# Kernel optimization log

Hardware: AMD Instinct MI355X
Metric: run time of the kernel (lower is better)

The kernel has to match this reference:

```python
import jax, jax.numpy as jnp
import numpy as np

D, E, H, K = 1024, 8, 1024, 2          # d_model, num_experts, hidden_size, top_k
NUM_LAYERS, LB_W, Z_W = 16, 0.01, 0.001
B, S = 2, 2048


def setup_inputs() -> dict:
    key = jax.random.key(0)
    ks = jax.random.split(key, 8)
    s = lambda d: 1.0 / np.sqrt(d)
    return {
        "x": jax.random.normal(ks[0], (B, S, D), jnp.float32),
        "w_router": jax.random.normal(ks[1], (D, E), jnp.float32) * s(D),
        "w1": jax.random.normal(ks[2], (E, D, H), jnp.float32) * s(D),
        "w3": jax.random.normal(ks[3], (E, D, H), jnp.float32) * s(D),
        "w2": jax.random.normal(ks[4], (E, H, D), jnp.float32) * s(H),
        "sw1": jax.random.normal(ks[5], (D, H), jnp.float32) * s(D),
        "sw3": jax.random.normal(ks[6], (D, H), jnp.float32) * s(D),
        "sw2": jax.random.normal(ks[7], (H, D), jnp.float32) * s(H),
    }


def reference(x, w_router, w1, w3, w2, sw1, sw3, sw2):
    b, s_len, _ = x.shape
    xt = x.reshape(-1, D)                       # (N, D) flattened tokens
    n_tok = xt.shape[0]

    # ---- router: softmax over experts, then top-k ----
    logits = xt @ w_router                      # (N, E)
    probs = jax.nn.softmax(logits, axis=-1)
    weights, indices = jax.lax.top_k(probs, K)  # (N, K)

    # combine weights scattered back to dense (N, E) form
    onehot = jax.nn.one_hot(indices, E, dtype=x.dtype)    # (N, K, E)
    cw = jnp.einsum("nk,nke->ne", weights, onehot)       # (N, E)
    counts = jnp.sum(onehot, axis=(0, 1))                 # (E,) tokens per expert

    # ---- expert SwiGLU MLPs (dense dispatch, weighted combine) ----
    g = jnp.einsum("nd,edh->neh", xt, w1)                 # (N, E, H)
    u = jnp.einsum("nd,edh->neh", xt, w3)
    h = jax.nn.silu(g) * u
    eout = jnp.einsum("neh,ehd->ned", h, w2)              # (N, E, D)
    out = jnp.einsum("ne,ned->nd", cw, eout)              # (N, D)

    # ---- shared expert, weighted-sum combine with top_k ----
    shared = (jax.nn.silu(xt @ sw1) * (xt @ sw3)) @ sw2   # (N, D)
    out = (out * K + shared) / (K + 1)

    # ---- aux losses (training mode) ----
    logits32 = logits.astype(jnp.float32)
    scale = E * LB_W / (NUM_LAYERS * n_tok * K)
    lb_loss = scale * jnp.dot(counts.astype(jnp.float32),
                              jax.nn.softmax(logits32, axis=-1).sum(axis=0))
    z_loss = jnp.mean(jnp.square(jax.nn.logsumexp(logits32, axis=-1))) * Z_W

    return out.reshape(b, s_len, D), lb_loss, z_loss
```

## Files before the change

### kernel.cpp

```cpp
#include <hip/hip_runtime.h>

#define NTOK 4096
#define NEXP 8
#define MAXTILES 104

typedef __attribute__((ext_vector_type(8))) short short8;
typedef __attribute__((ext_vector_type(4))) float f32x4;
typedef __attribute__((ext_vector_type(4))) unsigned int uint4v;
typedef __attribute__((ext_vector_type(2))) unsigned int uint2v;

__device__ __forceinline__ unsigned short f2bf(float f) {
  union { float f; unsigned u; } v; v.f = f;
  unsigned u = v.u;
  return (unsigned short)((u + 0x7FFFu + ((u >> 16) & 1u)) >> 16);
}

__device__ __forceinline__ void gll16(const void* g, void* l) {
  __builtin_amdgcn_global_load_lds((const __attribute__((address_space(1))) void*)g,
                                   (__attribute__((address_space(3))) void*)l, 16, 0, 0);
}

__device__ __forceinline__ void transpose_tile(const float* __restrict__ S,
                                               unsigned short* __restrict__ Dp,
                                               int r0, int c0, int t,
                                               unsigned short (*tile)[65]) {
  int r = t >> 2, cb = (t & 3) * 16;
  const float* sp = S + (size_t)(r0 + r) * 1024 + c0 + cb;
  f32x4 v0 = ((const f32x4*)sp)[0], v1 = ((const f32x4*)sp)[1];
  f32x4 v2 = ((const f32x4*)sp)[2], v3 = ((const f32x4*)sp)[3];
#pragma unroll
  for (int j = 0; j < 4; ++j) {
    tile[r][cb + j] = f2bf(v0[j]);
    tile[r][cb + 4 + j] = f2bf(v1[j]);
    tile[r][cb + 8 + j] = f2bf(v2[j]);
    tile[r][cb + 12 + j] = f2bf(v3[j]);
  }
  __syncthreads();
  unsigned short* dp = Dp + (size_t)(c0 + r) * 1024 + r0 + cb;
  uint4v o0, o1;
#pragma unroll
  for (int j = 0; j < 4; ++j) {
    o0[j] = (unsigned)tile[cb + 2 * j][r] | ((unsigned)tile[cb + 2 * j + 1][r] << 16);
    o1[j] = (unsigned)tile[cb + 8 + 2 * j][r] | ((unsigned)tile[cb + 9 + 2 * j][r] << 16);
  }
  ((uint4v*)dp)[0] = o0;
  ((uint4v*)dp)[1] = o1;
}

__global__ __launch_bounds__(256) void prep_k(
    const float* __restrict__ w1, const float* __restrict__ w3,
    const float* __restrict__ sw1, const float* __restrict__ sw3,
    unsigned short* __restrict__ dst ,
    const float* __restrict__ x, const float* __restrict__ wr, unsigned short* __restrict__ xb,
    int* __restrict__ rec, float* __restrict__ wts, float* __restrict__ probs,
    float* __restrict__ lsebuf) {
  __shared__ unsigned short tile[64][65];
  int b = blockIdx.x;
  if (b < 4608) {
    int z = b >> 8, rem = b & 255;
    const float* S;
    unsigned short* Dp;
    if (z < 8) { S = w1 + (size_t)z * 1048576; Dp = dst + (size_t)z * 1048576; }
    else if (z < 16) { S = w3 + (size_t)(z - 8) * 1048576; Dp = dst + (size_t)z * 1048576; }
    else if (z == 16) { S = sw1; Dp = dst + (size_t)24 * 1048576; }
    else { S = sw3; Dp = dst + (size_t)25 * 1048576; }
    transpose_tile(S, Dp, (rem >> 4) * 64, (rem & 15) * 64, threadIdx.x, tile);
  } else {
    int t = threadIdx.x, lane = t & 63, wv = t >> 6;
    int tok = (b - 4608) * 4 + wv;
    const f32x4* x4 = (const f32x4*)(x + (size_t)tok * 1024);
    f32x4 xv[4];
#pragma unroll
    for (int j = 0; j < 4; ++j) xv[j] = x4[j * 64 + lane];

    unsigned short* xo = xb + (size_t)tok * 1024;
#pragma unroll
    for (int j = 0; j < 4; ++j) {
      uint2v o;
      o[0] = (unsigned)f2bf(xv[j][0]) | ((unsigned)f2bf(xv[j][1]) << 16);
      o[1] = (unsigned)f2bf(xv[j][2]) | ((unsigned)f2bf(xv[j][3]) << 16);
      *(uint2v*)(xo + j * 256 + lane * 4) = o;
    }

    float acc[NEXP];
#pragma unroll
    for (int e = 0; e < NEXP; ++e) acc[e] = 0.f;
#pragma unroll
    for (int j = 0; j < 4; ++j) {
      int base = j * 256 + lane * 4;
#pragma unroll
      for (int c = 0; c < 4; ++c) {
        float xf = xv[j][c];
        const f32x4* wp = (const f32x4*)(wr + (size_t)(base + c) * NEXP);
        f32x4 q0 = wp[0], q1 = wp[1];
#pragma unroll
        for (int e = 0; e < 4; ++e) { acc[e] += xf * q0[e]; acc[4 + e] += xf * q1[e]; }
      }
    }
#pragma unroll
    for (int off = 32; off > 0; off >>= 1) {
#pragma unroll
      for (int e = 0; e < NEXP; ++e) acc[e] += __shfl_xor(acc[e], off);
    }

    float mx = acc[0];
#pragma unroll
    for (int e = 1; e < NEXP; ++e) mx = fmaxf(mx, acc[e]);
    float s = 0.f;
#pragma unroll
    for (int e = 0; e < NEXP; ++e) s += __expf(acc[e] - mx);
    float inv = 1.f / s;

    if (lane < NEXP) probs[(size_t)tok * NEXP + lane] = __expf(acc[lane] - mx) * inv;
    if (lane == 0) {
      int i0 = 0; float v0 = acc[0];
#pragma unroll
      for (int e = 1; e < NEXP; ++e) if (acc[e] > v0) { v0 = acc[e]; i0 = e; }
      int i1 = -1; float v1 = -3.4e38f;
#pragma unroll
      for (int e = 0; e < NEXP; ++e) if (e != i0 && acc[e] > v1) { v1 = acc[e]; i1 = e; }
      rec[tok] = i0 | (i1 << 8);
      wts[2 * tok] = __expf(v0 - mx) * inv;
      wts[2 * tok + 1] = __expf(v1 - mx) * inv;
      lsebuf[tok] = mx + __logf(s);
    }
  }
}

__global__ __launch_bounds__(1024) void build_k(
    const int* __restrict__ rec, const float* __restrict__ wts, const float* __restrict__ probs,
    const float* __restrict__ lsebuf,
    int* __restrict__ tlist, float* __restrict__ wlist,
    int* __restrict__ counts, int* __restrict__ ebase, int* __restrict__ tiles,
    float* __restrict__ lossout) {
  __shared__ int lcnt[NEXP];
  __shared__ float sprob[NEXP];
  __shared__ float sz;
  int t = threadIdx.x, lane = t & 63;
  if (t < NEXP) { lcnt[t] = 0; sprob[t] = 0.f; }
  if (t == 0) sz = 0.f;
  __syncthreads();

  float pacc[NEXP];
#pragma unroll
  for (int e = 0; e < NEXP; ++e) pacc[e] = 0.f;
  float zacc = 0.f;

#pragma unroll
  for (int it = 0; it < 4; ++it) {
    int tok = t + it * 1024;
    int r = rec[tok];
    int i0 = r & 255, i1 = (r >> 8) & 255;
    int p0 = atomicAdd(&lcnt[i0], 1);
    tlist[i0 * NTOK + p0] = tok;
    wlist[i0 * NTOK + p0] = wts[2 * tok];
    int p1 = atomicAdd(&lcnt[i1], 1);
    tlist[i1 * NTOK + p1] = tok | (1 << 16);
    wlist[i1 * NTOK + p1] = wts[2 * tok + 1];
    f32x4 a = ((const f32x4*)(probs + (size_t)tok * NEXP))[0];
    f32x4 c = ((const f32x4*)(probs + (size_t)tok * NEXP))[1];
#pragma unroll
    for (int j = 0; j < 4; ++j) { pacc[j] += a[j]; pacc[4 + j] += c[j]; }
    float lv = lsebuf[tok];
    zacc += lv * lv;
  }
#pragma unroll
  for (int off = 32; off > 0; off >>= 1) {
#pragma unroll
    for (int e = 0; e < NEXP; ++e) pacc[e] += __shfl_xor(pacc[e], off);
    zacc += __shfl_xor(zacc, off);
  }
  if (lane == 0) {
#pragma unroll
    for (int e = 0; e < NEXP; ++e) atomicAdd(&sprob[e], pacc[e]);
    atomicAdd(&sz, zacc);
  }
  __syncthreads();

  if (t == 0) {
    int a = 0, tt = 0;
    float dot = 0.f;
    for (int e = 0; e < NEXP; ++e) {
      counts[e] = lcnt[e];
      ebase[e] = a;
      int nt = (lcnt[e] + 127) >> 7;
      for (int i = 0; i < nt; ++i) tiles[tt++] = (e << 16) | i;
      a += nt * 128;
      dot += (float)lcnt[e] * sprob[e];
    }
    ebase[NEXP] = a;
    for (int i = 0; i < 32; ++i) tiles[tt++] = (NEXP << 16) | i;
    while (tt < MAXTILES) tiles[tt++] = -1;
    lossout[0] = 6.103515625e-7f * dot;
    lossout[1] = sz * (0.001f / 4096.f);
  }
}

__global__ __launch_bounds__(256, 3) void gemm1_k(
    const unsigned short* __restrict__ xb,
    const unsigned short* __restrict__ w1T, const unsigned short* __restrict__ w3T,
    const unsigned short* __restrict__ sw1T, const unsigned short* __restrict__ sw3T,
    unsigned short* __restrict__ hout,
    const int* __restrict__ tlist, const int* __restrict__ counts,
    const int* __restrict__ ebase, const int* __restrict__ tiles,
    const float* __restrict__ w2, const float* __restrict__ sw2,
    unsigned short* __restrict__ wTbase ) {
  __shared__ unsigned short As[128 * 64], Bs1[64 * 64], Bs3[64 * 64];
  const int tid = threadIdx.x;

  if (blockIdx.y >= MAXTILES) {
    int tb = (blockIdx.y - MAXTILES) * 16 + blockIdx.x;
    int z = tb >> 8, rem = tb & 255;
    const float* S = (z < 8) ? w2 + (size_t)z * 1048576 : sw2;
    unsigned short* Dp = (z < 8) ? wTbase + (size_t)(16 + z) * 1048576
                                 : wTbase + (size_t)26 * 1048576;
    transpose_tile(S, Dp, (rem >> 4) * 64, (rem & 15) * 64, tid,
                   (unsigned short (*)[65])As);
    return;
  }

  int td = tiles[blockIdx.y];
  if (td < 0) return;
  const int e = td >> 16;
  const int m0 = (td & 0xFFFF) << 7;
  const int n0 = blockIdx.x * 64;
  const bool sh = (e == NEXP);
  const int n_e = sh ? NTOK : counts[e];
  const int hb = ebase[e];
  const unsigned short* B1p = sh ? sw1T : w1T + (size_t)e * 1048576;
  const unsigned short* B3p = sh ? sw3T : w3T + (size_t)e * 1048576;
  const int* listp = tlist + e * NTOK;

  const int lane = tid & 63, wv = tid >> 6;
  const int wrw = wv >> 1, wc = wv & 1, l16 = lane & 15, lq = lane >> 4;

  const unsigned short* ga[4];
#pragma unroll
  for (int i = 0; i < 4; ++i) {
    int c = tid + i * 256;
    int r = c >> 3, ks = (c & 7) ^ (r & 7);
    int ar = m0 + r;
    int rowA = sh ? ar : (ar < n_e ? (listp[ar] & 0xFFFF) : 0);
    ga[i] = xb + (size_t)rowA * 1024 + ks * 8;
  }
  const unsigned short* gb[2];
  const unsigned short* gc[2];
#pragma unroll
  for (int i = 0; i < 2; ++i) {
    int c = tid + i * 256;
    int r = c >> 3, ks = (c & 7) ^ (r & 7);
    gb[i] = B1p + (size_t)(n0 + r) * 1024 + ks * 8;
    gc[i] = B3p + (size_t)(n0 + r) * 1024 + ks * 8;
  }
  unsigned short* lA[4];
#pragma unroll
  for (int i = 0; i < 4; ++i) lA[i] = As + i * 2048 + wv * 512;
  unsigned short* lB[2] = {Bs1 + wv * 512, Bs1 + 2048 + wv * 512};
  unsigned short* lC[2] = {Bs3 + wv * 512, Bs3 + 2048 + wv * 512};

  f32x4 accg[4][2], accu[4][2];
#pragma unroll
  for (int mi = 0; mi < 4; ++mi)
#pragma unroll
    for (int ni = 0; ni < 2; ++ni)
#pragma unroll
      for (int r = 0; r < 4; ++r) { accg[mi][ni][r] = 0.f; accu[mi][ni][r] = 0.f; }

  for (int k0 = 0; k0 < 1024; k0 += 64) {
#pragma unroll
    for (int i = 0; i < 4; ++i) { gll16(ga[i], lA[i]); ga[i] += 64; }
#pragma unroll
    for (int i = 0; i < 2; ++i) { gll16(gb[i], lB[i]); gb[i] += 64; gll16(gc[i], lC[i]); gc[i] += 64; }
    __syncthreads();
#pragma unroll
    for (int kh = 0; kh < 2; ++kh) {
      short8 af[4], b1f[2], b3f[2];
#pragma unroll
      for (int mi = 0; mi < 4; ++mi) {
        int R = wrw * 64 + mi * 16 + l16;
        int s = (kh * 4 + lq) ^ (R & 7);
        af[mi] = *(const short8*)&As[R * 64 + s * 8];
      }
#pragma unroll
      for (int ni = 0; ni < 2; ++ni) {
        int R = wc * 32 + ni * 16 + l16;
        int s = (kh * 4 + lq) ^ (R & 7);
        b1f[ni] = *(const short8*)&Bs1[R * 64 + s * 8];
        b3f[ni] = *(const short8*)&Bs3[R * 64 + s * 8];
      }
#pragma unroll
      for (int mi = 0; mi < 4; ++mi)
#pragma unroll
        for (int ni = 0; ni < 2; ++ni) {
          accg[mi][ni] = __builtin_amdgcn_mfma_f32_16x16x32_bf16(af[mi], b1f[ni], accg[mi][ni], 0, 0, 0);
          accu[mi][ni] = __builtin_amdgcn_mfma_f32_16x16x32_bf16(af[mi], b3f[ni], accu[mi][ni], 0, 0, 0);
        }
    }
    __syncthreads();
  }

#pragma unroll
  for (int mi = 0; mi < 4; ++mi)
#pragma unroll
    for (int ni = 0; ni < 2; ++ni) {
      int col = n0 + wc * 32 + ni * 16 + l16;
#pragma unroll
      for (int r = 0; r < 4; ++r) {
        int row = m0 + wrw * 64 + mi * 16 + lq * 4 + r;
        float g = accg[mi][ni][r], u = accu[mi][ni][r];
        float h = g / (1.f + __expf(-g)) * u;
        hout[(size_t)(hb + row) * 1024 + col] = (row < n_e) ? f2bf(h) : (unsigned short)0;
      }
    }
}

__global__ __launch_bounds__(256, 4) void gemm2_k(
    const unsigned short* __restrict__ hbuf,
    const unsigned short* __restrict__ w2T, const unsigned short* __restrict__ sw2T,
    float* __restrict__ ybuf, float* __restrict__ out,
    const int* __restrict__ tlist, const float* __restrict__ wlist,
    const int* __restrict__ counts, const int* __restrict__ ebase, const int* __restrict__ tiles) {
  int td = tiles[blockIdx.y];
  if (td < 0) return;
  const int e = td >> 16;
  const int m0 = (td & 0xFFFF) << 7;
  const int n0 = blockIdx.x * 64;
  const bool sh = (e == NEXP);
  const int n_e = sh ? NTOK : counts[e];
  const int hb = ebase[e];
  const unsigned short* Bp = sh ? sw2T : w2T + (size_t)e * 1048576;
  const int* listp = tlist + e * NTOK;

  __shared__ unsigned short As[128 * 64], Bs[64 * 64];
  const int tid = threadIdx.x, lane = tid & 63, wv = tid >> 6;
  const int wrw = wv >> 1, wc = wv & 1, l16 = lane & 15, lq = lane >> 4;

  const unsigned short* ga[4];
#pragma unroll
  for (int i = 0; i < 4; ++i) {
    int c = tid + i * 256;
    int r = c >> 3, ks = (c & 7) ^ (r & 7);
    ga[i] = hbuf + (size_t)(hb + m0 + r) * 1024 + ks * 8;
  }
  const unsigned short* gb[2];
#pragma unroll
  for (int i = 0; i < 2; ++i) {
    int c = tid + i * 256;
    int r = c >> 3, ks = (c & 7) ^ (r & 7);
    gb[i] = Bp + (size_t)(n0 + r) * 1024 + ks * 8;
  }
  unsigned short* lA[4];
#pragma unroll
  for (int i = 0; i < 4; ++i) lA[i] = As + i * 2048 + wv * 512;
  unsigned short* lB[2] = {Bs + wv * 512, Bs + 2048 + wv * 512};

  f32x4 acc[4][2];
#pragma unroll
  for (int mi = 0; mi < 4; ++mi)
#pragma unroll
    for (int ni = 0; ni < 2; ++ni)
#pragma unroll
      for (int r = 0; r < 4; ++r) acc[mi][ni][r] = 0.f;

  for (int k0 = 0; k0 < 1024; k0 += 64) {
#pragma unroll
    for (int i = 0; i < 4; ++i) { gll16(ga[i], lA[i]); ga[i] += 64; }
#pragma unroll
    for (int i = 0; i < 2; ++i) { gll16(gb[i], lB[i]); gb[i] += 64; }
    __syncthreads();
#pragma unroll
    for (int kh = 0; kh < 2; ++kh) {
      short8 af[4], bf[2];
#pragma unroll
      for (int mi = 0; mi < 4; ++mi) {
        int R = wrw * 64 + mi * 16 + l16;
        int s = (kh * 4 + lq) ^ (R & 7);
        af[mi] = *(const short8*)&As[R * 64 + s * 8];
      }
#pragma unroll
      for (int ni = 0; ni < 2; ++ni) {
        int R = wc * 32 + ni * 16 + l16;
        int s = (kh * 4 + lq) ^ (R & 7);
        bf[ni] = *(const short8*)&Bs[R * 64 + s * 8];
      }
#pragma unroll
      for (int mi = 0; mi < 4; ++mi)
#pragma unroll
        for (int ni = 0; ni < 2; ++ni)
          acc[mi][ni] = __builtin_amdgcn_mfma_f32_16x16x32_bf16(af[mi], bf[ni], acc[mi][ni], 0, 0, 0);
    }
    __syncthreads();
  }

#pragma unroll
  for (int mi = 0; mi < 4; ++mi)
#pragma unroll
    for (int r = 0; r < 4; ++r) {
      int row = m0 + wrw * 64 + mi * 16 + lq * 4 + r;
      int col = n0 + wc * 32 + l16;
      if (sh) {
        float* yp = out + (size_t)row * 1024 + col;
#pragma unroll
        for (int ni = 0; ni < 2; ++ni) yp[ni * 16] = acc[mi][ni][r] * (1.f / 3.f);
      } else if (row < n_e) {
        int ent = listp[row];
        float wt = wlist[e * NTOK + row] * (2.f / 3.f);
        int tok = ent & 0xFFFF, ks = ent >> 16;
        float* yp = ybuf + ((size_t)ks * NTOK + tok) * 1024 + col;
#pragma unroll
        for (int ni = 0; ni < 2; ++ni) yp[ni * 16] = wt * acc[mi][ni][r];
      }
    }
}

__global__ __launch_bounds__(256) void combine_k(const float* __restrict__ y,
                                                 float* __restrict__ out) {
  size_t i = (size_t)blockIdx.x * 256 + threadIdx.x;
  const f32x4* y0 = (const f32x4*)y + i;
  const f32x4* y1 = y0 + (NTOK * 1024 / 4);
  f32x4 o = ((f32x4*)out)[i];
  ((f32x4*)out)[i] = o + *y0 + *y1;
}

extern "C" void kernel_launch(void* const* d_in, const int* in_sizes, int n_in,
                              void* d_out, int out_size, void* d_ws, size_t ws_size,
                              hipStream_t stream) {
  const float* x   = (const float*)d_in[0];
  const float* wrt = (const float*)d_in[1];
  const float* w1  = (const float*)d_in[2];
  const float* w3  = (const float*)d_in[3];
  const float* w2  = (const float*)d_in[4];
  const float* sw1 = (const float*)d_in[5];
  const float* sw3 = (const float*)d_in[6];
  const float* sw2 = (const float*)d_in[7];
  float* out = (float*)d_out;

  char* p = (char*)d_ws;
  auto alloc = [&](size_t b) { char* r = p; p += (b + 255) & ~(size_t)255; return r; };
  unsigned short* xb   = (unsigned short*)alloc((size_t)NTOK * 1024 * 2);
  unsigned short* w1T  = (unsigned short*)alloc((size_t)27 * 1048576 * 2);
  unsigned short* w3T  = w1T + (size_t)8 * 1048576;
  unsigned short* w2T  = w3T + (size_t)8 * 1048576;
  unsigned short* sw1T = w2T + (size_t)8 * 1048576;
  unsigned short* sw3T = sw1T + 1048576;
  unsigned short* sw2T = sw3T + 1048576;
  unsigned short* hbuf = (unsigned short*)alloc((size_t)13312 * 1024 * 2);
  float* ybuf   = (float*)alloc((size_t)2 * NTOK * 1024 * 4);
  int* tlist    = (int*)alloc((size_t)NEXP * NTOK * 4);
  float* wlist  = (float*)alloc((size_t)NEXP * NTOK * 4);
  int* rec      = (int*)alloc((size_t)NTOK * 4);
  float* wts    = (float*)alloc((size_t)NTOK * 2 * 4);
  float* probs  = (float*)alloc((size_t)NTOK * NEXP * 4);
  float* lsebuf = (float*)alloc((size_t)NTOK * 4);
  int* tiles    = (int*)alloc(MAXTILES * 4);
  int* ebase    = (int*)alloc(256);
  int* counts   = (int*)alloc(256);

  prep_k<<<5632, 256, 0, stream>>>(w1, w3, sw1, sw3, w1T,
                                   x, wrt, xb, rec, wts, probs, lsebuf);
  build_k<<<1, 1024, 0, stream>>>(rec, wts, probs, lsebuf, tlist, wlist,
                                  counts, ebase, tiles, out + (size_t)NTOK * 1024);
  gemm1_k<<<dim3(16, MAXTILES + 144), 256, 0, stream>>>(
      xb, w1T, w3T, sw1T, sw3T, hbuf, tlist, counts, ebase, tiles, w2, sw2, w1T);
  gemm2_k<<<dim3(16, MAXTILES), 256, 0, stream>>>(hbuf, w2T, sw2T, ybuf, out,
                                                  tlist, wlist, counts, ebase, tiles);
  combine_k<<<NTOK * 1024 / 4 / 256, 256, 0, stream>>>(ybuf, out);
}
```

Measured before the change: 303.0 us.

## Eliminate single-block build kernel by doing routing scatter with global atomics

Removes the single-block build_k launch. Token routing lists are now built in prep_k with global atomics, GEMM kernels derive their tile assignment on the fly from the expert counts, and the aux-loss reduction moves into an extra block of combine_k. This drops a serialized one-block kernel and its launch gap, at the cost of a memset, global atomic contention on eight counters, and a per-block tile lookup loop. Token order within each expert list becomes nondeterministic.

After: 372.7 us. 23.0% more time.

```diff
diff --git a/kernel.cpp b/kernel.cpp
--- a/kernel.cpp
+++ b/kernel.cpp
@@ -18,6 +18,21 @@
 __device__ __forceinline__ void gll16(const void* g, void* l) {
   __builtin_amdgcn_global_load_lds((const __attribute__((address_space(1))) void*)g,
                                    (__attribute__((address_space(3))) void*)l, 16, 0, 0);
+}
+
+__device__ __forceinline__ bool tile_lookup(const int* __restrict__ counts, int y,
+                                            int& e, int& m0, int& n_e, int& hb) {
+  int base = 0, acc = 0;
+#pragma unroll
+  for (int ee = 0; ee < NEXP; ++ee) {
+    int c = counts[ee];
+    int nt = (c + 127) >> 7;
+    if (y < acc + nt) { e = ee; m0 = (y - acc) << 7; n_e = c; hb = base; return true; }
+    acc += nt; base += nt << 7;
+  }
+  int ys = y - acc;
+  if (ys < 32) { e = NEXP; m0 = ys << 7; n_e = NTOK; hb = base; return true; }
+  return false;
 }
 
 __device__ __forceinline__ void transpose_tile(const float* __restrict__ S,
@@ -52,8 +67,8 @@
     const float* __restrict__ sw1, const float* __restrict__ sw3,
     unsigned short* __restrict__ dst ,
     const float* __restrict__ x, const float* __restrict__ wr, unsigned short* __restrict__ xb,
-    int* __restrict__ rec, float* __restrict__ wts, float* __restrict__ probs,
-    float* __restrict__ lsebuf) {
+    int* __restrict__ counts, int* __restrict__ tlist, float* __restrict__ wlist,
+    float* __restrict__ probs, float* __restrict__ lsebuf) {
   __shared__ unsigned short tile[64][65];
   int b = blockIdx.x;
   if (b < 4608) {
@@ -119,80 +134,14 @@
       int i1 = -1; float v1 = -3.4e38f;
 #pragma unroll
       for (int e = 0; e < NEXP; ++e) if (e != i0 && acc[e] > v1) { v1 = acc[e]; i1 = e; }
-      rec[tok] = i0 | (i1 << 8);
-      wts[2 * tok] = __expf(v0 - mx) * inv;
-      wts[2 * tok + 1] = __expf(v1 - mx) * inv;
+      int p0 = atomicAdd(&counts[i0], 1);
+      tlist[i0 * NTOK + p0] = tok;
+      wlist[i0 * NTOK + p0] = __expf(v0 - mx) * inv;
+      int p1 = atomicAdd(&counts[i1], 1);
+      tlist[i1 * NTOK + p1] = tok | (1 << 16);
+      wlist[i1 * NTOK + p1] = __expf(v1 - mx) * inv;
       lsebuf[tok] = mx + __logf(s);
     }
-  }
-}
-
-__global__ __launch_bounds__(1024) void build_k(
-    const int* __restrict__ rec, const float* __restrict__ wts, const float* __restrict__ probs,
-    const float* __restrict__ lsebuf,
-    int* __restrict__ tlist, float* __restrict__ wlist,
-    int* __restrict__ counts, int* __restrict__ ebase, int* __restrict__ tiles,
-    float* __restrict__ lossout) {
-  __shared__ int lcnt[NEXP];
-  __shared__ float sprob[NEXP];
-  __shared__ float sz;
-  int t = threadIdx.x, lane = t & 63;
-  if (t < NEXP) { lcnt[t] = 0; sprob[t] = 0.f; }
-  if (t == 0) sz = 0.f;
-  __syncthreads();
-
-  float pacc[NEXP];
-#pragma unroll
-  for (int e = 0; e < NEXP; ++e) pacc[e] = 0.f;
-  float zacc = 0.f;
-
-#pragma unroll
-  for (int it = 0; it < 4; ++it) {
-    int tok = t + it * 1024;
-    int r = rec[tok];
-    int i0 = r & 255, i1 = (r >> 8) & 255;
-    int p0 = atomicAdd(&lcnt[i0], 1);
-    tlist[i0 * NTOK + p0] = tok;
-    wlist[i0 * NTOK + p0] = wts[2 * tok];
-    int p1 = atomicAdd(&lcnt[i1], 1);
-    tlist[i1 * NTOK + p1] = tok | (1 << 16);
-    wlist[i1 * NTOK + p1] = wts[2 * tok + 1];
-    f32x4 a = ((const f32x4*)(probs + (size_t)tok * NEXP))[0];
-    f32x4 c = ((const f32x4*)(probs + (size_t)tok * NEXP))[1];
-#pragma unroll
-    for (int j = 0; j < 4; ++j) { pacc[j] += a[j]; pacc[4 + j] += c[j]; }
-    float lv = lsebuf[tok];
-    zacc += lv * lv;
-  }
-#pragma unroll
-  for (int off = 32; off > 0; off >>= 1) {
-#pragma unroll
-    for (int e = 0; e < NEXP; ++e) pacc[e] += __shfl_xor(pacc[e], off);
-    zacc += __shfl_xor(zacc, off);
-  }
-  if (lane == 0) {
-#pragma unroll
-    for (int e = 0; e < NEXP; ++e) atomicAdd(&sprob[e], pacc[e]);
-    atomicAdd(&sz, zacc);
-  }
-  __syncthreads();
-
-  if (t == 0) {
-    int a = 0, tt = 0;
-    float dot = 0.f;
-    for (int e = 0; e < NEXP; ++e) {
-      counts[e] = lcnt[e];
-      ebase[e] = a;
-      int nt = (lcnt[e] + 127) >> 7;
-      for (int i = 0; i < nt; ++i) tiles[tt++] = (e << 16) | i;
-      a += nt * 128;
-      dot += (float)lcnt[e] * sprob[e];
-    }
-    ebase[NEXP] = a;
-    for (int i = 0; i < 32; ++i) tiles[tt++] = (NEXP << 16) | i;
-    while (tt < MAXTILES) tiles[tt++] = -1;
-    lossout[0] = 6.103515625e-7f * dot;
-    lossout[1] = sz * (0.001f / 4096.f);
   }
 }
 
@@ -202,7 +151,6 @@
     const unsigned short* __restrict__ sw1T, const unsigned short* __restrict__ sw3T,
     unsigned short* __restrict__ hout,
     const int* __restrict__ tlist, const int* __restrict__ counts,
-    const int* __restrict__ ebase, const int* __restrict__ tiles,
     const float* __restrict__ w2, const float* __restrict__ sw2,
     unsigned short* __restrict__ wTbase ) {
   __shared__ unsigned short As[128 * 64], Bs1[64 * 64], Bs3[64 * 64];
@@ -219,14 +167,10 @@
     return;
   }
 
-  int td = tiles[blockIdx.y];
-  if (td < 0) return;
-  const int e = td >> 16;
-  const int m0 = (td & 0xFFFF) << 7;
+  int e, m0, n_e, hb;
+  if (!tile_lookup(counts, blockIdx.y, e, m0, n_e, hb)) return;
   const int n0 = blockIdx.x * 64;
   const bool sh = (e == NEXP);
-  const int n_e = sh ? NTOK : counts[e];
-  const int hb = ebase[e];
   const unsigned short* B1p = sh ? sw1T : w1T + (size_t)e * 1048576;
   const unsigned short* B3p = sh ? sw3T : w3T + (size_t)e * 1048576;
   const int* listp = tlist + e * NTOK;
@@ -319,15 +263,11 @@
     const unsigned short* __restrict__ w2T, const unsigned short* __restrict__ sw2T,
     float* __restrict__ ybuf, float* __restrict__ out,
     const int* __restrict__ tlist, const float* __restrict__ wlist,
-    const int* __restrict__ counts, const int* __restrict__ ebase, const int* __restrict__ tiles) {
-  int td = tiles[blockIdx.y];
-  if (td < 0) return;
-  const int e = td >> 16;
-  const int m0 = (td & 0xFFFF) << 7;
+    const int* __restrict__ counts) {
+  int e, m0, n_e, hb;
+  if (!tile_lookup(counts, blockIdx.y, e, m0, n_e, hb)) return;
   const int n0 = blockIdx.x * 64;
   const bool sh = (e == NEXP);
-  const int n_e = sh ? NTOK : counts[e];
-  const int hb = ebase[e];
   const unsigned short* Bp = sh ? sw2T : w2T + (size_t)e * 1048576;
   const int* listp = tlist + e * NTOK;
 
@@ -414,12 +354,57 @@
 }
 
 __global__ __launch_bounds__(256) void combine_k(const float* __restrict__ y,
-                                                 float* __restrict__ out) {
-  size_t i = (size_t)blockIdx.x * 256 + threadIdx.x;
-  const f32x4* y0 = (const f32x4*)y + i;
-  const f32x4* y1 = y0 + (NTOK * 1024 / 4);
-  f32x4 o = ((f32x4*)out)[i];
-  ((f32x4*)out)[i] = o + *y0 + *y1;
+                                                 float* __restrict__ out,
+                                                 const float* __restrict__ probs,
+                                                 const float* __restrict__ lsebuf,
+                                                 const int* __restrict__ counts,
+                                                 float* __restrict__ lossout) {
+  if (blockIdx.x < NTOK * 1024 / 4 / 256) {
+    size_t i = (size_t)blockIdx.x * 256 + threadIdx.x;
+    const f32x4* y0 = (const f32x4*)y + i;
+    const f32x4* y1 = y0 + (NTOK * 1024 / 4);
+    f32x4 o = ((f32x4*)out)[i];
+    ((f32x4*)out)[i] = o + *y0 + *y1;
+    return;
+  }
+  int t = threadIdx.x, lane = t & 63, wv = t >> 6;
+  float pacc[NEXP];
+#pragma unroll
+  for (int e = 0; e < NEXP; ++e) pacc[e] = 0.f;
+  float zacc = 0.f;
+#pragma unroll
+  for (int it = 0; it < 16; ++it) {
+    int tok = t + it * 256;
+    f32x4 a = ((const f32x4*)(probs + (size_t)tok * NEXP))[0];
+    f32x4 c = ((const f32x4*)(probs + (size_t)tok * NEXP))[1];
+#pragma unroll
+    for (int j = 0; j < 4; ++j) { pacc[j] += a[j]; pacc[4 + j] += c[j]; }
+    float lv = lsebuf[tok];
+    zacc += lv * lv;
+  }
+#pragma unroll
+  for (int off = 32; off > 0; off >>= 1) {
+#pragma unroll
+    for (int e = 0; e < NEXP; ++e) pacc[e] += __shfl_xor(pacc[e], off);
+    zacc += __shfl_xor(zacc, off);
+  }
+  __shared__ float red[4][NEXP + 1];
+  if (lane == 0) {
+#pragma unroll
+    for (int e = 0; e < NEXP; ++e) red[wv][e] = pacc[e];
+    red[wv][NEXP] = zacc;
+  }
+  __syncthreads();
+  if (t == 0) {
+    float dot = 0.f, z = 0.f;
+    for (int e = 0; e < NEXP; ++e) {
+      float se = red[0][e] + red[1][e] + red[2][e] + red[3][e];
+      dot += (float)counts[e] * se;
+    }
+    z = red[0][NEXP] + red[1][NEXP] + red[2][NEXP] + red[3][NEXP];
+    lossout[0] = 6.103515625e-7f * dot;
+    lossout[1] = z * (0.001f / 4096.f);
+  }
 }
 
 extern "C" void kernel_launch(void* const* d_in, const int* in_sizes, int n_in,
@@ -448,21 +433,18 @@
   float* ybuf   = (float*)alloc((size_t)2 * NTOK * 1024 * 4);
   int* tlist    = (int*)alloc((size_t)NEXP * NTOK * 4);
   float* wlist  = (float*)alloc((size_t)NEXP * NTOK * 4);
-  int* rec      = (int*)alloc((size_t)NTOK * 4);
-  float* wts    = (float*)alloc((size_t)NTOK * 2 * 4);
   float* probs  = (float*)alloc((size_t)NTOK * NEXP * 4);
   float* lsebuf = (float*)alloc((size_t)NTOK * 4);
-  int* tiles    = (int*)alloc(MAXTILES * 4);
-  int* ebase    = (int*)alloc(256);
   int* counts   = (int*)alloc(256);
 
+  hipMemsetAsync(counts, 0, NEXP * 4, stream);
+
   prep_k<<<5632, 256, 0, stream>>>(w1, w3, sw1, sw3, w1T,
-                                   x, wrt, xb, rec, wts, probs, lsebuf);
-  build_k<<<1, 1024, 0, stream>>>(rec, wts, probs, lsebuf, tlist, wlist,
-                                  counts, ebase, tiles, out + (size_t)NTOK * 1024);
+                                   x, wrt, xb, counts, tlist, wlist, probs, lsebuf);
   gemm1_k<<<dim3(16, MAXTILES + 144), 256, 0, stream>>>(
-      xb, w1T, w3T, sw1T, sw3T, hbuf, tlist, counts, ebase, tiles, w2, sw2, w1T);
+      xb, w1T, w3T, sw1T, sw3T, hbuf, tlist, counts, w2, sw2, w1T);
   gemm2_k<<<dim3(16, MAXTILES), 256, 0, stream>>>(hbuf, w2T, sw2T, ybuf, out,
-                                                  tlist, wlist, counts, ebase, tiles);
-  combine_k<<<NTOK * 1024 / 4 / 256, 256, 0, stream>>>(ybuf, out);
-}
+                                                  tlist, wlist, counts);
+  combine_k<<<NTOK * 1024 / 4 / 256 + 1, 256, 0, stream>>>(
+      ybuf, out, probs, lsebuf, counts, out + (size_t)NTOK * 1024);
+}
```
